# Kernel tuning notes

Measured on AMD Instinct MI355X. Metric: run time of the kernel, lower is better.

The kernel has to match this reference:

```python
import jax, jax.numpy as jnp
import numpy as np

GAMMA = 0.9865
B, S, D = 8, 2048, 128


def setup_inputs() -> dict:
    key = jax.random.key(0)
    kq, kk, kv, kw = jax.random.split(key, 4)
    xq = jax.random.normal(kq, (B, S, D), dtype=jnp.float32)
    xk = jax.random.normal(kk, (B, S, D), dtype=jnp.float32)
    xv = jax.random.normal(kv, (B, S, D), dtype=jnp.float32)
    # NOTE: the original builds three Dense layers by repeating the SAME object,
    # so Q/K/V share a single no-bias weight matrix W.
    W = jax.random.normal(kw, (D, D), dtype=jnp.float32) * (1.0 / np.sqrt(D))
    return {"xq": xq, "xk": xk, "xv": xv, "W": W}


def _decay_matrix(seq_len, gamma):
    # Original: factors[i,j] = gamma^(i-j); keep upper triangle (j>=i); transpose.
    # Result: Dm[n,m] = gamma^(m-n) for n >= m, else 0 (lower triangular).
    n = jnp.arange(seq_len, dtype=jnp.float32)
    expo = n[None, :] - n[:, None]            # [S,S], entry (n,m) = m - n
    Dm = jnp.tril(jnp.float32(gamma) ** expo)  # zero out m > n before they'd matter
    return Dm


def reference(xq, xk, xv, W):
    Q = xq @ W
    K = xk @ W
    V = xv @ W
    d = Q.shape[-1]
    scores = jnp.einsum('bnd,bmd->bnm', Q, K) / jnp.sqrt(jnp.float32(d))
    Dm = _decay_matrix(Q.shape[1], GAMMA)
    # D /= reduce_sum(D, axis=1) ** 0.5  -> row-sums broadcast over LAST axis,
    # i.e. column m of D is divided by sqrt(rowsum[m]). Faithful to tf broadcasting.
    Dm = Dm / jnp.sqrt(jnp.sum(Dm, axis=1))
    scores = scores * Dm
    # per-batch norm: xs[n,m] / max(|sum_k xs[m,k]|, 1)  (tf broadcasting over last axis)
    s = jnp.sum(scores, axis=2)                       # [B,S]
    scores = scores / jnp.maximum(jnp.abs(s), 1.0)[:, None, :]
    return scores @ V
```

## Files before the change

### kernel.cpp

```cpp
#include <hip/hip_runtime.h>
#include <math.h>


constexpr int B = 8, S = 2048, D = 128;
constexpr int C = 64, NC = S / C;
constexpr int BS = B * S;
constexpr int NCH = B * NC;
#define GAMMA_F 0.9865f

typedef __attribute__((ext_vector_type(8))) short short8;
typedef __attribute__((ext_vector_type(8))) unsigned short ushort8;
typedef __attribute__((ext_vector_type(4))) float f32x4;

__device__ inline unsigned short f2bf(float f) {
  unsigned u = __builtin_bit_cast(unsigned, f);
  return (unsigned short)((u + 0x7FFF + ((u >> 16) & 1)) >> 16);
}
__device__ inline float bf2f(unsigned short h) {
  return __builtin_bit_cast(float, (unsigned)h << 16);
}

__global__ __launch_bounds__(128) void k_y(const float* __restrict__ xk,
                                           float* __restrict__ yc) {
  __shared__ float ksl[64];
  int bc = blockIdx.x, tid = threadIdx.x;
  float lgf = logf(GAMMA_F);
  if (tid < 64) {
    int n = (bc * 64 + tid) & (S - 1);
    float rs = (expf(-lgf * (float)(n + 1)) - 1.f) * (GAMMA_F / (1.f - GAMMA_F));
    ksl[tid] = expf(lgf * (float)n) / sqrtf(rs);
  }
  __syncthreads();
  const float* x = xk + (size_t)bc * 64 * 128 + tid;
  float a = 0.f;
#pragma unroll
  for (int j = 0; j < 64; j++) a = fmaf(ksl[j], x[j * 128], a);
  yc[(size_t)bc * 128 + tid] = a;
}

__global__ __launch_bounds__(1024, 1) void k_big(
    const float* __restrict__ xq, const float* __restrict__ xk,
    const float* __restrict__ xv, const float* __restrict__ W,
    const float* __restrict__ yc, unsigned short* __restrict__ qb,
    unsigned short* __restrict__ al, unsigned short* __restrict__ vbT,
    unsigned short* __restrict__ Hc) {
  __shared__ unsigned short qkv[3][64][136];
  __shared__ alignas(16) char ovl[36864];
  __shared__ float csp[128];
  __shared__ float ysum[128];
  __shared__ float cspp[8][128];
  __shared__ float invl[64];
  __shared__ float rsum_l[4][64];
  auto wt = (unsigned short(*)[136])ovl;
  auto kT = (unsigned short(*)[72])ovl;
  auto vT = (unsigned short(*)[72])(ovl + 18432);

  int bc = blockIdx.x, b = bc >> 5, c = bc & 31;
  int tid = threadIdx.x, w = tid >> 6, lane = tid & 63;
  int l15 = lane & 15, kg = (lane >> 4) * 8;
  float lgf = logf(GAMMA_F);

  for (int idx = tid; idx < 128 * 128; idx += 1024) {
    int cc = idx >> 7, k = idx & 127;
    wt[cc][k] = f2bf(W[k * 128 + cc]);
  }
  if (tid < 128) {
    float a = 0.f;
    for (int cc = 0; cc < c; cc++) a += yc[(size_t)(b * NC + cc) * 128 + tid];
    ysum[tid] = a;
  }
  __syncthreads();

  {
    int rt = w & 3, cq = w >> 2;
    int arow = rt * 16 + l15;
    size_t grow = (size_t)(bc * 64 + arow) * 128;
    for (int mat = 0; mat < 3; mat++) {
      const float* X = (mat == 0) ? xq : ((mat == 1) ? xk : xv);
      f32x4 acc[2];
#pragma unroll
      for (int j = 0; j < 2; j++) acc[j] = (f32x4){0.f, 0.f, 0.f, 0.f};
#pragma unroll
      for (int t = 0; t < 4; t++) {
        int k0 = t * 32 + kg;
        const float* ap = X + grow + k0;
        float a8[8];
        *(f32x4*)(a8) = *(const f32x4*)ap;
        *(f32x4*)(a8 + 4) = *(const f32x4*)(ap + 4);
        short8 af;
#pragma unroll
        for (int i = 0; i < 8; i++) af[i] = (short)f2bf(a8[i]);
#pragma unroll
        for (int j = 0; j < 2; j++) {
          short8 bf = *(const short8*)&wt[(cq * 2 + j) * 16 + l15][k0];
          acc[j] = __builtin_amdgcn_mfma_f32_16x16x32_bf16(af, bf, acc[j], 0, 0, 0);
        }
      }
      int crow = rt * 16 + (lane >> 4) * 4;
#pragma unroll
      for (int rr = 0; rr < 4; rr++) {
        int row = crow + rr;
        int n = (bc * 64 + row) & (S - 1);
        float sc;
        if (mat == 0) {
          sc = expf(-lgf * (float)n) * 0.088388347f;
        } else if (mat == 1) {
          float rs = (expf(-lgf * (float)(n + 1)) - 1.f) * (GAMMA_F / (1.f - GAMMA_F));
          sc = expf(lgf * (float)n) / sqrtf(rs);
        } else {
          sc = 1.f;
        }
#pragma unroll
        for (int j = 0; j < 2; j++)
          qkv[mat][row][(cq * 2 + j) * 16 + l15] = f2bf(acc[j][rr] * sc);
      }
    }
  }
  {
    int d = tid & 127, q = tid >> 7;
    float part = 0.f;
#pragma unroll
    for (int k = 0; k < 16; k++)
      part = fmaf(ysum[16 * q + k], bf2f(wt[d][16 * q + k]), part);
    cspp[q][d] = part;
  }
  __syncthreads();

  if (tid < 128) {
    float a = 0.f;
#pragma unroll
    for (int q = 0; q < 8; q++) a += cspp[q][tid];
    csp[tid] = a;
  }
  {
    int row = tid >> 4, col = (tid & 15) * 8;
    *(ushort8*)(qb + (size_t)(bc * 64 + row) * 128 + col) =
        *(const ushort8*)&qkv[0][row][col];
  }
  {
    int rt2 = w & 3, mt = w >> 2;
    int arow = rt2 * 16 + l15;
    int crow = rt2 * 16 + (lane >> 4) * 4;
    f32x4 a1 = (f32x4){0.f, 0.f, 0.f, 0.f};
#pragma unroll
    for (int t = 0; t < 4; t++) {
      int k0 = t * 32 + kg;
      short8 af = *(const short8*)&qkv[0][arow][k0];
      short8 bf = *(const short8*)&qkv[1][mt * 16 + l15][k0];
      a1 = __builtin_amdgcn_mfma_f32_16x16x32_bf16(af, bf, a1, 0, 0, 0);
    }
    unsigned short* alg = al + (size_t)bc * 64 * 64;
    float rsp[4];
#pragma unroll
    for (int rr = 0; rr < 4; rr++) {
      int n_l = crow + rr, m_l = mt * 16 + l15;
      float mv = (n_l >= m_l) ? a1[rr] : 0.f;
      alg[n_l * 64 + m_l] = f2bf(mv);
      rsp[rr] = mv;
    }
#pragma unroll
    for (int rr = 0; rr < 4; rr++) {
      float r = rsp[rr];
      r += __shfl_xor(r, 1); r += __shfl_xor(r, 2);
      r += __shfl_xor(r, 4); r += __shfl_xor(r, 8);
      if (l15 == 0) rsum_l[mt][crow + rr] = r;
    }
  }
  {
    int d = tid & 127, g8 = tid >> 7;
    ushort8 pk;
#pragma unroll
    for (int i = 0; i < 8; i++) pk[i] = qkv[1][g8 * 8 + i][d];
    *(ushort8*)&kT[d][g8 * 8] = pk;
  }
  {
    int d = tid & 127, g8 = tid >> 7;
    ushort8 pk;
#pragma unroll
    for (int i = 0; i < 8; i++) pk[i] = qkv[2][g8 * 8 + i][d];
    *(ushort8*)&vT[d][g8 * 8] = pk;
  }
  __syncthreads();

  {
    int row = tid >> 4, part = tid & 15;
    ushort8 q8 = *(const ushort8*)&qkv[0][row][part * 8];
    float dot = 0.f;
#pragma unroll
    for (int ii = 0; ii < 8; ii++) dot = fmaf(bf2f(q8[ii]), csp[part * 8 + ii], dot);
    dot += __shfl_xor(dot, 1); dot += __shfl_xor(dot, 2);
    dot += __shfl_xor(dot, 4); dot += __shfl_xor(dot, 8);
    if (part == 0) {
      float s = rsum_l[0][row] + rsum_l[1][row] + rsum_l[2][row] + rsum_l[3][row] + dot;
      invl[row] = 1.f / fmaxf(fabsf(s), 1.f);
    }
  }
  __syncthreads();

  {
    int d = tid >> 3, ms = (tid & 7) * 8;
    ushort8 v8 = *(const ushort8*)&vT[d][ms];
    ushort8 o;
#pragma unroll
    for (int ii = 0; ii < 8; ii++) o[ii] = f2bf(bf2f(v8[ii]) * invl[ms + ii]);
    *(ushort8*)&vT[d][ms] = o;
  }
  __syncthreads();

  {
    int d2t = w >> 1, jh = w & 1;
    f32x4 hacc[4];
#pragma unroll
    for (int j = 0; j < 4; j++) hacc[j] = (f32x4){0.f, 0.f, 0.f, 0.f};
#pragma unroll
    for (int t = 0; t < 2; t++) {
      int k0 = t * 32 + kg;
      short8 a2 = *(const short8*)&vT[d2t * 16 + l15][k0];
#pragma unroll
      for (int j = 0; j < 4; j++) {
        short8 bf = *(const short8*)&kT[(jh * 4 + j) * 16 + l15][k0];
        hacc[j] = __builtin_amdgcn_mfma_f32_16x16x32_bf16(a2, bf, hacc[j], 0, 0, 0);
      }
    }
    unsigned short* g = Hc + (size_t)bc * D * D;
#pragma unroll
    for (int j = 0; j < 4; j++)
#pragma unroll
      for (int rr = 0; rr < 4; rr++)
        g[(size_t)(d2t * 16 + (lane >> 4) * 4 + rr) * D + (jh * 4 + j) * 16 + l15] =
            f2bf(hacc[j][rr]);
  }
  {
    int d = tid >> 3, pp = (tid & 7) * 8;
    *(ushort8*)(vbT + (size_t)bc * D * C + (size_t)d * C + pp) =
        *(const ushort8*)&vT[d][pp];
  }
}

__global__ __launch_bounds__(1024, 1) void k_out2(
    const unsigned short* __restrict__ qb, const unsigned short* __restrict__ al,
    const unsigned short* __restrict__ vbT, const unsigned short* __restrict__ Hc,
    float* __restrict__ out) {
  __shared__ unsigned short SEL[128][136];
  int bc = blockIdx.x, b = bc >> 5, c = bc & 31;
  int tid = threadIdx.x, w = tid >> 6, lane = tid & 63;
  int l15 = lane & 15, kg = (lane >> 4) * 8;

  {
    int slot = tid * 16;
    int r = slot >> 7, col = slot & 127;
    float accf[16];
#pragma unroll
    for (int i = 0; i < 16; i++) accf[i] = 0.f;
    const unsigned short* base = Hc + (size_t)(b * NC) * D * D + (size_t)r * D + col;
    for (int cc = 0; cc < c; cc++) {
      ushort8 v0 = *(const ushort8*)(base + (size_t)cc * D * D);
      ushort8 v1 = *(const ushort8*)(base + (size_t)cc * D * D + 8);
#pragma unroll
      for (int i = 0; i < 8; i++) {
        accf[i] += bf2f(v0[i]);
        accf[8 + i] += bf2f(v1[i]);
      }
    }
    ushort8 o0, o1;
#pragma unroll
    for (int i = 0; i < 8; i++) { o0[i] = f2bf(accf[i]); o1[i] = f2bf(accf[8 + i]); }
    *(ushort8*)&SEL[r][col] = o0;
    *(ushort8*)&SEL[r][col + 8] = o1;
  }
  __syncthreads();

  size_t base = (size_t)bc * C * D;
  int rt = w & 3, ch = w >> 2;
  int arow = rt * 16 + l15;
  int crow = rt * 16 + (lane >> 4) * 4;

  f32x4 acc[2];
#pragma unroll
  for (int j = 0; j < 2; j++) acc[j] = (f32x4){0.f, 0.f, 0.f, 0.f};
#pragma unroll
  for (int t = 0; t < 4; t++) {
    int k0 = t * 32 + kg;
    short8 af = *(const short8*)(qb + base + (size_t)arow * D + k0);
#pragma unroll
    for (int jj = 0; jj < 2; jj++) {
      short8 bf = *(const short8*)&SEL[(ch * 2 + jj) * 16 + l15][k0];
      acc[jj] = __builtin_amdgcn_mfma_f32_16x16x32_bf16(af, bf, acc[jj], 0, 0, 0);
    }
  }
  const unsigned short* alg = al + (size_t)bc * 64 * 64;
  const unsigned short* vt = vbT + (size_t)bc * D * C;
#pragma unroll
  for (int t = 0; t < 2; t++) {
    int k0 = t * 32 + kg;
    short8 af = *(const short8*)(alg + (size_t)arow * 64 + k0);
#pragma unroll
    for (int jj = 0; jj < 2; jj++) {
      short8 bf = *(const short8*)(vt + (size_t)((ch * 2 + jj) * 16 + l15) * C + k0);
      acc[jj] = __builtin_amdgcn_mfma_f32_16x16x32_bf16(af, bf, acc[jj], 0, 0, 0);
    }
  }
#pragma unroll
  for (int jj = 0; jj < 2; jj++)
#pragma unroll
    for (int rr = 0; rr < 4; rr++)
      out[base + (size_t)(crow + rr) * D + (ch * 2 + jj) * 16 + l15] = acc[jj][rr];
}

extern "C" void kernel_launch(void* const* d_in, const int* in_sizes, int n_in,
                              void* d_out, int out_size, void* d_ws, size_t ws_size,
                              hipStream_t stream) {
  const float* xq = (const float*)d_in[0];
  const float* xk = (const float*)d_in[1];
  const float* xv = (const float*)d_in[2];
  const float* W  = (const float*)d_in[3];
  float* out = (float*)d_out;

  char* p = (char*)d_ws;
  float* yc = (float*)p;                     p += (size_t)NCH * D * 4;
  unsigned short* qb  = (unsigned short*)p;  p += (size_t)BS * D * 2;
  unsigned short* al  = (unsigned short*)p;  p += (size_t)NCH * C * C * 2;
  unsigned short* vbT = (unsigned short*)p;  p += (size_t)NCH * D * C * 2;
  unsigned short* Hc  = (unsigned short*)p;  p += (size_t)NCH * D * D * 2;

  hipLaunchKernelGGL(k_y, dim3(NCH), dim3(128), 0, stream, xk, yc);
  hipLaunchKernelGGL(k_big, dim3(NCH), dim3(1024), 0, stream,
                     xq, xk, xv, W, yc, qb, al, vbT, Hc);
  hipLaunchKernelGGL(k_out2, dim3(NCH), dim3(1024), 0, stream, qb, al, vbT, Hc, out);
}
```

Before: 61.10 us.

## Replace per-block serial prefix of chunk states with parallel scan kernel

Weight transpose/bf16 conversion moves into extra blocks of the first kernel, so each k_big block no longer redoes it, and k_big reads W from global memory. K and V transposes are written straight from MFMA accumulators, which drops a separate shared-memory transpose pass and a barrier. The O(c) per-block summation of previous chunk states in the output kernel is replaced by a dedicated prefix-scan kernel over chunks, and the output kernel is split across twice as many smaller blocks. This adds a kernel launch and an extra workspace buffer of scanned states in exchange for removing redundant serial reads.

```diff
diff --git a/kernel.cpp b/kernel.cpp
--- a/kernel.cpp
+++ b/kernel.cpp
@@ -10,6 +10,7 @@
 
 typedef __attribute__((ext_vector_type(8))) short short8;
 typedef __attribute__((ext_vector_type(8))) unsigned short ushort8;
+typedef __attribute__((ext_vector_type(4))) unsigned short bf4;
 typedef __attribute__((ext_vector_type(4))) float f32x4;
 
 __device__ inline unsigned short f2bf(float f) {
@@ -21,59 +22,64 @@
 }
 
 __global__ __launch_bounds__(128) void k_y(const float* __restrict__ xk,
-                                           float* __restrict__ yc) {
+                                           const float* __restrict__ W,
+                                           float* __restrict__ yc,
+                                           unsigned short* __restrict__ wtg) {
+  int bid = blockIdx.x, tid = threadIdx.x;
+  if (bid >= NCH) {
+    int e0 = (bid - NCH) * 256 + tid;
+#pragma unroll
+    for (int h = 0; h < 2; h++) {
+      int e = e0 + h * 128;
+      int c = e >> 7, k = e & 127;
+      wtg[c * 128 + k] = f2bf(W[k * 128 + c]);
+    }
+    return;
+  }
   __shared__ float ksl[64];
-  int bc = blockIdx.x, tid = threadIdx.x;
   float lgf = logf(GAMMA_F);
   if (tid < 64) {
-    int n = (bc * 64 + tid) & (S - 1);
+    int n = (bid * 64 + tid) & (S - 1);
     float rs = (expf(-lgf * (float)(n + 1)) - 1.f) * (GAMMA_F / (1.f - GAMMA_F));
     ksl[tid] = expf(lgf * (float)n) / sqrtf(rs);
   }
   __syncthreads();
-  const float* x = xk + (size_t)bc * 64 * 128 + tid;
+  const float* x = xk + (size_t)bid * 64 * 128 + tid;
   float a = 0.f;
 #pragma unroll
   for (int j = 0; j < 64; j++) a = fmaf(ksl[j], x[j * 128], a);
-  yc[(size_t)bc * 128 + tid] = a;
+  yc[(size_t)bid * 128 + tid] = a;
 }
 
 __global__ __launch_bounds__(1024, 1) void k_big(
     const float* __restrict__ xq, const float* __restrict__ xk,
-    const float* __restrict__ xv, const float* __restrict__ W,
+    const float* __restrict__ xv, const unsigned short* __restrict__ wtg,
     const float* __restrict__ yc, unsigned short* __restrict__ qb,
     unsigned short* __restrict__ al, unsigned short* __restrict__ vbT,
     unsigned short* __restrict__ Hc) {
-  __shared__ unsigned short qkv[3][64][136];
-  __shared__ alignas(16) char ovl[36864];
-  __shared__ float csp[128];
+  __shared__ unsigned short qkv[2][64][136];
+  __shared__ unsigned short kT[128][72];
+  __shared__ unsigned short vT[128][72];
+  __shared__ float cspp[8][128];
   __shared__ float ysum[128];
-  __shared__ float cspp[8][128];
   __shared__ float invl[64];
   __shared__ float rsum_l[4][64];
-  auto wt = (unsigned short(*)[136])ovl;
-  auto kT = (unsigned short(*)[72])ovl;
-  auto vT = (unsigned short(*)[72])(ovl + 18432);
 
   int bc = blockIdx.x, b = bc >> 5, c = bc & 31;
   int tid = threadIdx.x, w = tid >> 6, lane = tid & 63;
   int l15 = lane & 15, kg = (lane >> 4) * 8;
   float lgf = logf(GAMMA_F);
 
-  for (int idx = tid; idx < 128 * 128; idx += 1024) {
-    int cc = idx >> 7, k = idx & 127;
-    wt[cc][k] = f2bf(W[k * 128 + cc]);
-  }
   if (tid < 128) {
     float a = 0.f;
     for (int cc = 0; cc < c; cc++) a += yc[(size_t)(b * NC + cc) * 128 + tid];
     ysum[tid] = a;
   }
-  __syncthreads();
 
   {
     int rt = w & 3, cq = w >> 2;
     int arow = rt * 16 + l15;
+    int crow = rt * 16 + (lane >> 4) * 4;
     size_t grow = (size_t)(bc * 64 + arow) * 128;
     for (int mat = 0; mat < 3; mat++) {
       const float* X = (mat == 0) ? xq : ((mat == 1) ? xk : xv);
@@ -92,15 +98,14 @@
         for (int i = 0; i < 8; i++) af[i] = (short)f2bf(a8[i]);
 #pragma unroll
         for (int j = 0; j < 2; j++) {
-          short8 bf = *(const short8*)&wt[(cq * 2 + j) * 16 + l15][k0];
+          short8 bf = *(const short8*)(wtg + (size_t)((cq * 2 + j) * 16 + l15) * 128 + k0);
           acc[j] = __builtin_amdgcn_mfma_f32_16x16x32_bf16(af, bf, acc[j], 0, 0, 0);
         }
       }
-      int crow = rt * 16 + (lane >> 4) * 4;
+      float sv[2][4];
 #pragma unroll
       for (int rr = 0; rr < 4; rr++) {
-        int row = crow + rr;
-        int n = (bc * 64 + row) & (S - 1);
+        int n = (bc * 64 + crow + rr) & (S - 1);
         float sc;
         if (mat == 0) {
           sc = expf(-lgf * (float)n) * 0.088388347f;
@@ -111,26 +116,44 @@
           sc = 1.f;
         }
 #pragma unroll
-        for (int j = 0; j < 2; j++)
-          qkv[mat][row][(cq * 2 + j) * 16 + l15] = f2bf(acc[j][rr] * sc);
-      }
-    }
-  }
+        for (int j = 0; j < 2; j++) sv[j][rr] = acc[j][rr] * sc;
+      }
+      if (mat < 2) {
+#pragma unroll
+        for (int rr = 0; rr < 4; rr++)
+#pragma unroll
+          for (int j = 0; j < 2; j++)
+            qkv[mat][crow + rr][(cq * 2 + j) * 16 + l15] = f2bf(sv[j][rr]);
+      }
+      if (mat == 1) {
+#pragma unroll
+        for (int j = 0; j < 2; j++) {
+          bf4 pk;
+#pragma unroll
+          for (int rr = 0; rr < 4; rr++) pk[rr] = f2bf(sv[j][rr]);
+          *(bf4*)&kT[(cq * 2 + j) * 16 + l15][crow] = pk;
+        }
+      }
+      if (mat == 2) {
+#pragma unroll
+        for (int j = 0; j < 2; j++) {
+          bf4 pk;
+#pragma unroll
+          for (int rr = 0; rr < 4; rr++) pk[rr] = f2bf(sv[j][rr]);
+          *(bf4*)&vT[(cq * 2 + j) * 16 + l15][crow] = pk;
+        }
+      }
+    }
+  }
+  __syncthreads();
+
   {
     int d = tid & 127, q = tid >> 7;
+    const unsigned short* wr = wtg + (size_t)d * 128 + q * 16;
     float part = 0.f;
 #pragma unroll
-    for (int k = 0; k < 16; k++)
-      part = fmaf(ysum[16 * q + k], bf2f(wt[d][16 * q + k]), part);
+    for (int k = 0; k < 16; k++) part = fmaf(ysum[q * 16 + k], bf2f(wr[k]), part);
     cspp[q][d] = part;
-  }
-  __syncthreads();
-
-  if (tid < 128) {
-    float a = 0.f;
-#pragma unroll
-    for (int q = 0; q < 8; q++) a += cspp[q][tid];
-    csp[tid] = a;
   }
   {
     int row = tid >> 4, col = (tid & 15) * 8;
@@ -166,20 +189,6 @@
       if (l15 == 0) rsum_l[mt][crow + rr] = r;
     }
   }
-  {
-    int d = tid & 127, g8 = tid >> 7;
-    ushort8 pk;
-#pragma unroll
-    for (int i = 0; i < 8; i++) pk[i] = qkv[1][g8 * 8 + i][d];
-    *(ushort8*)&kT[d][g8 * 8] = pk;
-  }
-  {
-    int d = tid & 127, g8 = tid >> 7;
-    ushort8 pk;
-#pragma unroll
-    for (int i = 0; i < 8; i++) pk[i] = qkv[2][g8 * 8 + i][d];
-    *(ushort8*)&vT[d][g8 * 8] = pk;
-  }
   __syncthreads();
 
   {
@@ -187,7 +196,12 @@
     ushort8 q8 = *(const ushort8*)&qkv[0][row][part * 8];
     float dot = 0.f;
 #pragma unroll
-    for (int ii = 0; ii < 8; ii++) dot = fmaf(bf2f(q8[ii]), csp[part * 8 + ii], dot);
+    for (int ii = 0; ii < 8; ii++) {
+      int kk = part * 8 + ii;
+      float csum = cspp[0][kk] + cspp[1][kk] + cspp[2][kk] + cspp[3][kk] +
+                   cspp[4][kk] + cspp[5][kk] + cspp[6][kk] + cspp[7][kk];
+      dot = fmaf(bf2f(q8[ii]), csum, dot);
+    }
     dot += __shfl_xor(dot, 1); dot += __shfl_xor(dot, 2);
     dot += __shfl_xor(dot, 4); dot += __shfl_xor(dot, 8);
     if (part == 0) {
@@ -237,54 +251,70 @@
   }
 }
 
-__global__ __launch_bounds__(1024, 1) void k_out2(
+__global__ __launch_bounds__(256) void k_gscan(const unsigned short* __restrict__ Hc,
+                                               unsigned short* __restrict__ HS) {
+  __shared__ float ttot[4][64][8];
+  int b = blockIdx.x, gy = blockIdx.y;
+  int tid = threadIdx.x, g = tid >> 6, slot = tid & 63;
+  int d2 = gy * 4 + (slot >> 4), d1 = (slot & 15) * 8;
+  size_t off = ((size_t)(b * NC) * D + d2) * D + d1;
+  ushort8 v[8];
+  float tot[8];
+#pragma unroll
+  for (int j = 0; j < 8; j++) tot[j] = 0.f;
+#pragma unroll
+  for (int i = 0; i < 8; i++) {
+    v[i] = *(const ushort8*)(Hc + off + (size_t)(g * 8 + i) * D * D);
+#pragma unroll
+    for (int j = 0; j < 8; j++) tot[j] += bf2f(v[i][j]);
+  }
+#pragma unroll
+  for (int j = 0; j < 8; j++) ttot[g][slot][j] = tot[j];
+  __syncthreads();
+  float run[8];
+#pragma unroll
+  for (int j = 0; j < 8; j++) run[j] = 0.f;
+  for (int gg = 0; gg < 4; gg++)
+    if (gg < g)
+#pragma unroll
+      for (int j = 0; j < 8; j++) run[j] += ttot[gg][slot][j];
+#pragma unroll
+  for (int i = 0; i < 8; i++) {
+    ushort8 o;
+#pragma unroll
+    for (int j = 0; j < 8; j++) {
+      o[j] = f2bf(run[j]);
+      run[j] += bf2f(v[i][j]);
+    }
+    *(ushort8*)(HS + off + (size_t)(g * 8 + i) * D * D) = o;
+  }
+}
+
+__global__ __launch_bounds__(512) void k_out(
     const unsigned short* __restrict__ qb, const unsigned short* __restrict__ al,
-    const unsigned short* __restrict__ vbT, const unsigned short* __restrict__ Hc,
+    const unsigned short* __restrict__ vbT, const unsigned short* __restrict__ HS,
     float* __restrict__ out) {
-  __shared__ unsigned short SEL[128][136];
-  int bc = blockIdx.x, b = bc >> 5, c = bc & 31;
+  int bc = blockIdx.x, ch2 = blockIdx.y;
   int tid = threadIdx.x, w = tid >> 6, lane = tid & 63;
-  int l15 = lane & 15, kg = (lane >> 4) * 8;
-
-  {
-    int slot = tid * 16;
-    int r = slot >> 7, col = slot & 127;
-    float accf[16];
-#pragma unroll
-    for (int i = 0; i < 16; i++) accf[i] = 0.f;
-    const unsigned short* base = Hc + (size_t)(b * NC) * D * D + (size_t)r * D + col;
-    for (int cc = 0; cc < c; cc++) {
-      ushort8 v0 = *(const ushort8*)(base + (size_t)cc * D * D);
-      ushort8 v1 = *(const ushort8*)(base + (size_t)cc * D * D + 8);
-#pragma unroll
-      for (int i = 0; i < 8; i++) {
-        accf[i] += bf2f(v0[i]);
-        accf[8 + i] += bf2f(v1[i]);
-      }
-    }
-    ushort8 o0, o1;
-#pragma unroll
-    for (int i = 0; i < 8; i++) { o0[i] = f2bf(accf[i]); o1[i] = f2bf(accf[8 + i]); }
-    *(ushort8*)&SEL[r][col] = o0;
-    *(ushort8*)&SEL[r][col + 8] = o1;
-  }
-  __syncthreads();
-
+  int l15 = lane & 15;
   size_t base = (size_t)bc * C * D;
-  int rt = w & 3, ch = w >> 2;
+  int kg = (lane >> 4) * 8;
+  int rt = w >> 1, chw = w & 1;
   int arow = rt * 16 + l15;
   int crow = rt * 16 + (lane >> 4) * 4;
 
   f32x4 acc[2];
 #pragma unroll
   for (int j = 0; j < 2; j++) acc[j] = (f32x4){0.f, 0.f, 0.f, 0.f};
+  const unsigned short* hrow = HS + (size_t)bc * D * D;
 #pragma unroll
   for (int t = 0; t < 4; t++) {
     int k0 = t * 32 + kg;
     short8 af = *(const short8*)(qb + base + (size_t)arow * D + k0);
 #pragma unroll
     for (int jj = 0; jj < 2; jj++) {
-      short8 bf = *(const short8*)&SEL[(ch * 2 + jj) * 16 + l15][k0];
+      int j = ch2 * 4 + chw * 2 + jj;
+      short8 bf = *(const short8*)(hrow + (size_t)(j * 16 + l15) * D + k0);
       acc[jj] = __builtin_amdgcn_mfma_f32_16x16x32_bf16(af, bf, acc[jj], 0, 0, 0);
     }
   }
@@ -296,7 +326,8 @@
     short8 af = *(const short8*)(alg + (size_t)arow * 64 + k0);
 #pragma unroll
     for (int jj = 0; jj < 2; jj++) {
-      short8 bf = *(const short8*)(vt + (size_t)((ch * 2 + jj) * 16 + l15) * C + k0);
+      int j = ch2 * 4 + chw * 2 + jj;
+      short8 bf = *(const short8*)(vt + (size_t)(j * 16 + l15) * C + k0);
       acc[jj] = __builtin_amdgcn_mfma_f32_16x16x32_bf16(af, bf, acc[jj], 0, 0, 0);
     }
   }
@@ -304,7 +335,8 @@
   for (int jj = 0; jj < 2; jj++)
 #pragma unroll
     for (int rr = 0; rr < 4; rr++)
-      out[base + (size_t)(crow + rr) * D + (ch * 2 + jj) * 16 + l15] = acc[jj][rr];
+      out[base + (size_t)(crow + rr) * D + (ch2 * 4 + chw * 2 + jj) * 16 + l15] =
+          acc[jj][rr];
 }
 
 extern "C" void kernel_launch(void* const* d_in, const int* in_sizes, int n_in,
@@ -318,13 +350,16 @@
 
   char* p = (char*)d_ws;
   float* yc = (float*)p;                     p += (size_t)NCH * D * 4;
+  unsigned short* wtg = (unsigned short*)p;  p += (size_t)D * D * 2;
   unsigned short* qb  = (unsigned short*)p;  p += (size_t)BS * D * 2;
   unsigned short* al  = (unsigned short*)p;  p += (size_t)NCH * C * C * 2;
   unsigned short* vbT = (unsigned short*)p;  p += (size_t)NCH * D * C * 2;
   unsigned short* Hc  = (unsigned short*)p;  p += (size_t)NCH * D * D * 2;
-
-  hipLaunchKernelGGL(k_y, dim3(NCH), dim3(128), 0, stream, xk, yc);
+  unsigned short* HS  = (unsigned short*)p;  p += (size_t)NCH * D * D * 2;
+
+  hipLaunchKernelGGL(k_y, dim3(NCH + 64), dim3(128), 0, stream, xk, W, yc, wtg);
   hipLaunchKernelGGL(k_big, dim3(NCH), dim3(1024), 0, stream,
-                     xq, xk, xv, W, yc, qb, al, vbT, Hc);
-  hipLaunchKernelGGL(k_out2, dim3(NCH), dim3(1024), 0, stream, qb, al, vbT, Hc, out);
-}
+                     xq, xk, xv, wtg, yc, qb, al, vbT, Hc);
+  hipLaunchKernelGGL(k_gscan, dim3(B, 32), dim3(256), 0, stream, Hc, HS);
+  hipLaunchKernelGGL(k_out, dim3(NCH, 2), dim3(512), 0, stream, qb, al, vbT, HS, out);
+}
```

Result: faster. 57.63 us (-5.7%).
